# Kernel tuning notes

Hardware: AMD Instinct MI355X
Metric: run time of the kernel (lower is better)

Reference implementation:

```python
import jax, jax.numpy as jnp
import numpy as np

NUM_SECTORS = 11


def setup_inputs() -> dict:
    key = jax.random.key(0)
    k0, k1, k2, k3 = jax.random.split(key, 4)
    B, N, C, H = 4, 2048, 512, 8
    x = jax.random.normal(k0, (B, N, C), dtype=jnp.float32)
    w_qkv = jax.random.normal(k1, (C, 3 * C), dtype=jnp.float32) * 0.02
    w_proj = jax.random.normal(k2, (C, C), dtype=jnp.float32) * 0.02
    b_proj = jnp.zeros((C,), dtype=jnp.float32)
    gate_logit = jnp.full((H,), 2.0, dtype=jnp.float32)
    sector_ids = jax.random.randint(k3, (N,), 0, NUM_SECTORS, dtype=jnp.int64)
    return {"x": x, "w_qkv": w_qkv, "w_proj": w_proj, "b_proj": b_proj,
            "gate_logit": gate_logit, "sector_ids": sector_ids}


def reference(x, w_qkv, w_proj, b_proj, gate_logit, sector_ids):
    B, N, C = x.shape
    H = gate_logit.shape[0]
    d = C // H
    scale = d ** -0.5

    qkv = (x @ w_qkv).reshape(B, N, 3, H, d)
    qkv = jnp.transpose(qkv, (2, 0, 3, 1, 4))  # (3, B, H, N, d)
    q, k, v = qkv[0], qkv[1], qkv[2]

    # Content attention: softmax(QK^T / sqrt(d)) @ V
    attn = jnp.einsum('bhnd,bhmd->bhnm', q, k) * scale
    attn = jax.nn.softmax(attn, axis=-1)
    v_content = jnp.einsum('bhnm,bhmd->bhnd', attn, v)

    # Positional path: A_pos @ V == per-sector mean of V, gathered per row.
    # A_pos[i,j] = 1/|sector(i)| if sector(i)==sector(j); row_sum >= 1 always.
    ids = sector_ids.astype(jnp.int32)
    counts = jax.ops.segment_sum(jnp.ones((N,), x.dtype), ids, num_segments=NUM_SECTORS)
    counts = jnp.maximum(counts, 1.0)
    v_nfirst = jnp.transpose(v, (2, 0, 1, 3)).reshape(N, B * H * d)  # (N, BHd)
    sums = jax.ops.segment_sum(v_nfirst, ids, num_segments=NUM_SECTORS)  # (S, BHd)
    means = sums / counts[:, None]
    v_pos = means[ids].reshape(N, B, H, d).transpose(1, 2, 0, 3)  # (B, H, N, d)

    g = jax.nn.sigmoid(gate_logit)[None, :, None, None]
    out = g * v_pos + (1.0 - g) * v_content  # (B, H, N, d)
    out = jnp.transpose(out, (0, 2, 1, 3)).reshape(B, N, C)
    return out @ w_proj + b_proj
```

## Files before the change

kernel.cpp:

```cpp
#include <hip/hip_runtime.h>
#include <hip/hip_bf16.h>
#include <stdint.h>

typedef float f32x4 __attribute__((ext_vector_type(4)));
typedef float f32x16 __attribute__((ext_vector_type(16)));
typedef short bf16x8 __attribute__((ext_vector_type(8)));
typedef short short4v __attribute__((ext_vector_type(4)));
typedef int i32x4 __attribute__((ext_vector_type(4)));

#define MFMA16(a, b, c) __builtin_amdgcn_mfma_f32_16x16x32_bf16(a, b, c, 0, 0, 0)
#define MFMA32(a, b, c) __builtin_amdgcn_mfma_f32_32x32x16_bf16(a, b, c, 0, 0, 0)

__device__ __forceinline__ float bf2f(unsigned short u) {
    unsigned int x = ((unsigned int)u) << 16;
    float f;
    __builtin_memcpy(&f, &x, 4);
    return f;
}
__device__ __forceinline__ unsigned short f2bf(float f) {
    unsigned int x;
    __builtin_memcpy(&x, &f, 4);
    unsigned int r = x + 0x7FFFu + ((x >> 16) & 1u);
    return (unsigned short)(r >> 16);
}
__device__ __forceinline__ unsigned int cvt_pk_bf16(float lo, float hi) {
    unsigned int d;
    asm("v_cvt_pk_bf16_f32 %0, %1, %2" : "=v"(d) : "v"(lo), "v"(hi));
    return d;
}

#define GLD16(g, l)                                                        \
    __builtin_amdgcn_global_load_lds(                                      \
        (const __attribute__((address_space(1))) void*)(g),                \
        (__attribute__((address_space(3))) void*)(l), 16, 0, 0)

#define QSCALE 0.18033688011112042f

__global__ __launch_bounds__(256) void k_cvt_x(const float* __restrict__ x,
                                               unsigned short* __restrict__ xb) {
    int i = (blockIdx.x * 256 + threadIdx.x) * 4;
    float4 v = *(const float4*)(x + i);
    short4v o;
    o.x = (short)f2bf(v.x);
    o.y = (short)f2bf(v.y);
    o.z = (short)f2bf(v.z);
    o.w = (short)f2bf(v.w);
    *(short4v*)(xb + i) = o;
}

__global__ __launch_bounds__(256) void k_transpose_bf16(const float* __restrict__ in,
                                                        unsigned short* __restrict__ out,
                                                        int R, int C) {
    __shared__ float tile[32][33];
    int tx = threadIdx.x & 31, ty = threadIdx.x >> 5;
    int r0 = blockIdx.y * 32, c0 = blockIdx.x * 32;
#pragma unroll
    for (int i = 0; i < 32; i += 8) tile[ty + i][tx] = in[(r0 + ty + i) * C + c0 + tx];
    __syncthreads();
#pragma unroll
    for (int i = 0; i < 32; i += 8) out[(c0 + ty + i) * R + r0 + tx] = f2bf(tile[tx][ty + i]);
}

__global__ __launch_bounds__(256) void k_gemm_qkv(const unsigned short* __restrict__ A,
                                                  const unsigned short* __restrict__ Bt,
                                                  unsigned short* __restrict__ Q,
                                                  unsigned short* __restrict__ Kd,
                                                  unsigned short* __restrict__ Vt) {
    __shared__ alignas(16) unsigned short smem[128 * 128];
    unsigned short* As = smem;
    unsigned short* Bs = smem + 128 * 64;
    const int t = threadIdx.x;
    const int w = t >> 6, l = t & 63;
    const int brow = blockIdx.x * 128, bcol = blockIdx.y * 128;
    const int wr = (w >> 1) * 64, wc = (w & 1) * 64;
    const int li = l & 15, lk = (l >> 4) * 8;
    f32x4 acc[4][4] = {};

    for (int kt = 0; kt < 512; kt += 64) {
#pragma unroll
        for (int i = 0; i < 4; i++) {
            int ub = i * 256 + w * 64;
            int r = (ub >> 3) + (l >> 3);
            int ck = l & 7;
            GLD16(A + (brow + r) * 512 + kt + ck * 8, As + ub * 8);
            GLD16(Bt + (bcol + r) * 512 + kt + ck * 8, Bs + ub * 8);
        }
        __syncthreads();
#pragma unroll
        for (int ks = 0; ks < 2; ks++) {
            bf16x8 af[4], bfr[4];
#pragma unroll
            for (int m = 0; m < 4; m++)
                af[m] = *(const bf16x8*)(As + (wr + m * 16 + li) * 64 + ks * 32 + lk);
#pragma unroll
            for (int n = 0; n < 4; n++)
                bfr[n] = *(const bf16x8*)(Bs + (wc + n * 16 + li) * 64 + ks * 32 + lk);
#pragma unroll
            for (int m = 0; m < 4; m++)
#pragma unroll
                for (int n = 0; n < 4; n++)
                    acc[m][n] = MFMA16(af[m], bfr[n], acc[m][n]);
        }
        __syncthreads();
    }

    const int bb = brow >> 11, tok0 = brow & 2047;
    if (bcol < 1024) {
#pragma unroll
        for (int m = 0; m < 4; m++) {
#pragma unroll
            for (int n = 0; n < 4; n++) {
#pragma unroll
                for (int r = 0; r < 4; r++) {
                    int gm = brow + wr + m * 16 + (l >> 4) * 4 + r;
                    int gn = bcol + wc + n * 16 + li;
                    float v = acc[m][n][r];
                    int tok = gm & 2047;
                    int three = gn >> 9, hh = (gn >> 6) & 7, dd = gn & 63;
                    int bh = bb * 8 + hh;
                    if (three == 0)
                        Q[((bh << 11) + tok) * 64 + dd] = f2bf(v * QSCALE);
                    else
                        Kd[((bh << 11) + tok) * 64 + dd] = f2bf(v);
                }
            }
        }
    } else {
#pragma unroll
        for (int m = 0; m < 4; m++) {
#pragma unroll
            for (int n = 0; n < 4; n++) {
#pragma unroll
                for (int r = 0; r < 4; r++) {
                    int gnl = wc + n * 16 + li;
                    int gml = wr + m * 16 + (l >> 4) * 4 + r;
                    smem[gnl * 128 + (gml ^ ((gnl & 7) << 3))] = f2bf(acc[m][n][r]);
                }
            }
        }
        __syncthreads();
        int gnl = t >> 1, half = t & 1;
        int vcol = (bcol - 1024) + gnl;
        int hh = (vcol >> 6) & 7, dd = vcol & 63;
        unsigned short* dst = Vt + ((size_t)((bb * 8 + hh) * 64 + dd) << 11) + tok0 + half * 64;
#pragma unroll
        for (int j = 0; j < 8; j++) {
            int elem = (half * 64 + j * 8) ^ ((gnl & 7) << 3);
            *(bf16x8*)(dst + j * 8) = *(const bf16x8*)&smem[gnl * 128 + elem];
        }
    }
}

__global__ __launch_bounds__(256, 4) void k_attn(const unsigned short* __restrict__ Q,
                                                 const unsigned short* __restrict__ K,
                                                 const unsigned short* __restrict__ Vt,
                                                 const float* __restrict__ sums,
                                                 const float* __restrict__ invc,
                                                 const int* __restrict__ ids,
                                                 const float* __restrict__ gate,
                                                 unsigned short* __restrict__ mixb) {
    __shared__ alignas(16) unsigned short Ks[3][64 * 64];
    __shared__ alignas(16) unsigned short Vs[2][64 * 64];
    const int bid = blockIdx.x;
    const int bh = bid >> 5, qb = bid & 31;
    const int w = threadIdx.x >> 6, l = threadIdx.x & 63;
    const int wq = w >> 1, wk = w & 1;
    const int q = l & 31, hi = l >> 5;
    const unsigned short* Qh = Q + (size_t)bh * 2048 * 64;
    const char* Kb = (const char*)(K + (size_t)bh * 2048 * 64);
    const char* Vb = (const char*)(Vt + (size_t)bh * 64 * 2048);
    const int qbase = qb * 64 + wq * 32;
    const int swz = (q & 7) << 4;

    bf16x8 qf[4];
#pragma unroll
    for (int ks = 0; ks < 4; ks++)
        qf[ks] = *(const bf16x8*)(Qh + (qbase + q) * 64 + ks * 16 + hi * 8);

    f32x16 o0 = {}, o1 = {};
    float mx = -1e30f, sm = 0.f;

    auto stageK = [&](int buf, int kt) {
#pragma unroll
        for (int i = 0; i < 2; i++) {
            int abase = (w * 2 + i) * 1024;
            int al = abase + l * 16;
            int g = al ^ (((al >> 7) & 7) << 4);
            GLD16(Kb + (size_t)kt * 128 + g, (char*)Ks[buf] + abase);
        }
    };
    auto stageV = [&](int buf, int kt) {
#pragma unroll
        for (int i = 0; i < 2; i++) {
            int abase = (w * 2 + i) * 1024;
            int al = abase + l * 16;
            int row = al >> 7;
            int col = (al & 127) ^ ((row & 7) << 4);
            GLD16(Vb + (size_t)row * 4096 + kt * 2 + col, (char*)Vs[buf] + abase);
        }
    };

    stageK(0, 0);
    stageV(0, 0);
    stageK(1, 64);

#pragma unroll 1
    for (int it = 0; it < 32; ++it) {
        if (it < 31)
            asm volatile("s_waitcnt vmcnt(2)" ::: "memory");
        else
            asm volatile("s_waitcnt vmcnt(0)" ::: "memory");
        __builtin_amdgcn_sched_barrier(0);
        __builtin_amdgcn_s_barrier();
        __builtin_amdgcn_sched_barrier(0);

        if (it < 31) stageV((it + 1) & 1, (it + 1) * 64);
        __builtin_amdgcn_sched_barrier(0);
        if (it < 30) stageK((it + 2) % 3, (it + 2) * 64);

        const char* Kc = (const char*)Ks[it % 3];
        f32x16 s0 = {};
        __builtin_amdgcn_s_setprio(1);
#pragma unroll
        for (int ks = 0; ks < 4; ks++) {
            bf16x8 kf = *(const bf16x8*)(Kc + (wk * 32 + q) * 128 + ((ks * 32 + hi * 16) ^ swz));
            s0 = MFMA32(kf, qf[ks], s0);
        }
        __builtin_amdgcn_s_setprio(0);

        float c8[8];
#pragma unroll
        for (int r = 0; r < 8; r++) c8[r] = fmaxf(s0[r], s0[r + 8]);
#pragma unroll
        for (int r = 0; r < 4; r++) c8[r] = fmaxf(c8[r], c8[r + 4]);
        float tm = fmaxf(fmaxf(c8[0], c8[1]), fmaxf(c8[2], c8[3]));

        if (!__all(tm <= mx + 8.0f)) {
            float tmf = fmaxf(tm, __shfl_xor(tm, 32));
            float mn = fmaxf(mx, tmf);
            float fac = __builtin_amdgcn_exp2f(mx - mn);
            mx = mn;
#pragma unroll
            for (int r = 0; r < 16; r++) {
                o0[r] *= fac;
                o1[r] *= fac;
            }
            sm *= fac;
        }

        float a0 = 0.f, a1 = 0.f, a2 = 0.f, a3 = 0.f;
#pragma unroll
        for (int r = 0; r < 16; r += 4) {
            float p0 = __builtin_amdgcn_exp2f(s0[r] - mx);
            float p1 = __builtin_amdgcn_exp2f(s0[r + 1] - mx);
            float p2 = __builtin_amdgcn_exp2f(s0[r + 2] - mx);
            float p3 = __builtin_amdgcn_exp2f(s0[r + 3] - mx);
            s0[r] = p0;
            s0[r + 1] = p1;
            s0[r + 2] = p2;
            s0[r + 3] = p3;
            a0 += p0;
            a1 += p1;
            a2 += p2;
            a3 += p3;
        }
        sm += (a0 + a1) + (a2 + a3);

        unsigned int pk[4][2];
#pragma unroll
        for (int aa = 0; aa < 4; aa++)
#pragma unroll
            for (int c = 0; c < 2; c++)
                pk[aa][c] = cvt_pk_bf16(s0[4 * aa + 2 * c], s0[4 * aa + 2 * c + 1]);

        const char* Vc = (const char*)Vs[it & 1];
        __builtin_amdgcn_s_setprio(1);
#pragma unroll
        for (int ksl = 0; ksl < 2; ksl++) {
            unsigned int send0 = hi ? pk[2 * ksl][0] : pk[2 * ksl + 1][0];
            unsigned int send1 = hi ? pk[2 * ksl][1] : pk[2 * ksl + 1][1];
            unsigned int r0 = (unsigned int)__shfl_xor((int)send0, 32);
            unsigned int r1 = (unsigned int)__shfl_xor((int)send1, 32);
            unsigned int u0 = hi ? r0 : pk[2 * ksl][0];
            unsigned int u1 = hi ? r1 : pk[2 * ksl][1];
            unsigned int u2 = hi ? pk[2 * ksl + 1][0] : r0;
            unsigned int u3 = hi ? pk[2 * ksl + 1][1] : r1;
            i32x4 uu = {(int)u0, (int)u1, (int)u2, (int)u3};
            bf16x8 pa = __builtin_bit_cast(bf16x8, uu);
            int vcol = (wk * 64 + ksl * 32 + hi * 16);
            bf16x8 vf0 = *(const bf16x8*)(Vc + q * 128 + (vcol ^ swz));
            bf16x8 vf1 = *(const bf16x8*)(Vc + (q + 32) * 128 + (vcol ^ swz));
            o0 = MFMA32(pa, vf0, o0);
            o1 = MFMA32(pa, vf1, o1);
        }
        __builtin_amdgcn_s_setprio(0);
    }

    __syncthreads();

    sm = sm + __shfl_xor(sm, 32);

    float* So = ((float*)Ks) + wq * 2048;
    float* Sml = ((float*)Vs) + wq * 128;
    if (wk == 1) {
#pragma unroll
        for (int r = 0; r < 16; r++) {
            So[r * 64 + l] = o0[r];
            So[(16 + r) * 64 + l] = o1[r];
        }
        Sml[l] = mx;
        Sml[64 + l] = sm;
    }
    __syncthreads();
    if (wk == 0) {
        float m1 = Sml[l], l1 = Sml[64 + l];
        float ms = fmaxf(mx, m1);
        float f0 = __builtin_amdgcn_exp2f(mx - ms);
        float f1 = __builtin_amdgcn_exp2f(m1 - ms);
        float inv = 1.f / (f0 * sm + f1 * l1);
        float g = 1.f / (1.f + __expf(-gate[bh & 7]));
        float omg = 1.f - g;
        unsigned short* mrow = mixb + (size_t)(bh >> 3) * 2048 * 512 + (bh & 7) * 64;
#pragma unroll
        for (int r = 0; r < 16; r++) {
            float om0 = f0 * o0[r] + f1 * So[r * 64 + l];
            float om1 = f0 * o1[r] + f1 * So[(16 + r) * 64 + l];
            int qq = (r & 3) + 8 * (r >> 2) + 4 * hi;
            float iv = __shfl(inv, qq);
            int tok = qbase + qq;
            int sid = ids[tok];
            float ic = invc[sid];
            float vp0 = sums[((sid * 32 + bh) << 6) + q];
            float vp1 = sums[((sid * 32 + bh) << 6) + q + 32];
            mrow[(size_t)tok * 512 + q] = f2bf(g * vp0 * ic + omg * om0 * iv);
            mrow[(size_t)tok * 512 + q + 32] = f2bf(g * vp1 * ic + omg * om1 * iv);
        }
    }
}

__global__ void k_counts(const int* __restrict__ ids, float* __restrict__ invc) {
    __shared__ float h[11];
    int t = threadIdx.x;
    if (t < 11) h[t] = 0.f;
    __syncthreads();
    for (int n = t; n < 2048; n += 256) atomicAdd(&h[ids[n]], 1.0f);
    __syncthreads();
    if (t < 11) invc[t] = 1.f / fmaxf(h[t], 1.f);
}

__global__ __launch_bounds__(256) void k_sums(const unsigned short* __restrict__ Vt,
                                              const int* __restrict__ ids,
                                              float* __restrict__ sums) {
    __shared__ int ids_s[512];
    int bh = blockIdx.x, ch = blockIdx.y;
    int t = threadIdx.x;
    ids_s[t] = ids[ch * 512 + t];
    ids_s[t + 256] = ids[ch * 512 + 256 + t];
    __syncthreads();
    int dd = t & 63, sub = t >> 6;
    const unsigned short* row = Vt + ((size_t)(bh * 64 + dd) << 11) + ch * 512 + sub * 128;
    const int* idp = ids_s + sub * 128;
    float acc[11] = {};
    for (int i = 0; i < 128; i++) {
        float v = bf2f(row[i]);
        int s = idp[i];
#pragma unroll
        for (int si = 0; si < 11; si++) acc[si] += (s == si) ? v : 0.f;
    }
#pragma unroll
    for (int si = 0; si < 11; si++) atomicAdd(&sums[((si * 32 + bh) << 6) + dd], acc[si]);
}

__global__ __launch_bounds__(256) void k_gemm_out(const unsigned short* __restrict__ A,
                                                  const unsigned short* __restrict__ Bt,
                                                  const float* __restrict__ bias,
                                                  float* __restrict__ out) {
    __shared__ alignas(16) unsigned short As[64 * 64];
    __shared__ alignas(16) unsigned short Bs[128 * 64];
    const int t = threadIdx.x;
    const int w = t >> 6, l = t & 63;
    const int brow = blockIdx.x * 64, bcol = blockIdx.y * 128;
    const int wc = w * 32;
    const int li = l & 15, lk = (l >> 4) * 8;
    f32x4 acc[4][2] = {};

    for (int kt = 0; kt < 512; kt += 64) {
#pragma unroll
        for (int i = 0; i < 2; i++) {
            int ub = i * 256 + w * 64;
            int r = (ub >> 3) + (l >> 3);
            int ck = l & 7;
            GLD16(A + (brow + r) * 512 + kt + ck * 8, As + ub * 8);
        }
#pragma unroll
        for (int i = 0; i < 4; i++) {
            int ub = i * 256 + w * 64;
            int r = (ub >> 3) + (l >> 3);
            int ck = l & 7;
            GLD16(Bt + (bcol + r) * 512 + kt + ck * 8, Bs + ub * 8);
        }
        __syncthreads();
#pragma unroll
        for (int ks = 0; ks < 2; ks++) {
            bf16x8 af[4], bfr[2];
#pragma unroll
            for (int m = 0; m < 4; m++)
                af[m] = *(const bf16x8*)(As + (m * 16 + li) * 64 + ks * 32 + lk);
#pragma unroll
            for (int n = 0; n < 2; n++)
                bfr[n] = *(const bf16x8*)(Bs + (wc + n * 16 + li) * 64 + ks * 32 + lk);
#pragma unroll
            for (int m = 0; m < 4; m++)
#pragma unroll
                for (int n = 0; n < 2; n++)
                    acc[m][n] = MFMA16(af[m], bfr[n], acc[m][n]);
        }
        __syncthreads();
    }
#pragma unroll
    for (int m = 0; m < 4; m++) {
#pragma unroll
        for (int n = 0; n < 2; n++) {
#pragma unroll
            for (int r = 0; r < 4; r++) {
                int gm = brow + m * 16 + (l >> 4) * 4 + r;
                int gn = bcol + wc + n * 16 + li;
                out[(size_t)gm * 512 + gn] = acc[m][n][r] + bias[gn];
            }
        }
    }
}

extern "C" void kernel_launch(void* const* d_in, const int* in_sizes, int n_in,
                              void* d_out, int out_size, void* d_ws, size_t ws_size,
                              hipStream_t stream) {
    const float* x = (const float*)d_in[0];
    const float* w_qkv = (const float*)d_in[1];
    const float* w_proj = (const float*)d_in[2];
    const float* b_proj = (const float*)d_in[3];
    const float* gate = (const float*)d_in[4];
    const int* ids = (const int*)d_in[5];
    float* out = (float*)d_out;
    char* ws = (char*)d_ws;

    unsigned short* xb = (unsigned short*)(ws + 0);
    unsigned short* wqT = (unsigned short*)(ws + 8388608);
    unsigned short* wpT = (unsigned short*)(ws + 9961472);
    unsigned short* Q = (unsigned short*)(ws + 10485760);
    unsigned short* Kd = (unsigned short*)(ws + 18874368);
    unsigned short* Vt = (unsigned short*)(ws + 27262976);
    float* sums = (float*)(ws + 52428800);
    float* invc = (float*)(ws + 52518912);
    unsigned short* mixb = xb;

    hipMemsetAsync(ws + 52428800, 0, 90112 + 64, stream);

    k_cvt_x<<<4096, 256, 0, stream>>>(x, xb);
    {
        dim3 g(48, 16);
        k_transpose_bf16<<<g, 256, 0, stream>>>(w_qkv, wqT, 512, 1536);
    }
    {
        dim3 g(16, 16);
        k_transpose_bf16<<<g, 256, 0, stream>>>(w_proj, wpT, 512, 512);
    }
    {
        dim3 g(64, 12);
        k_gemm_qkv<<<g, 256, 0, stream>>>(xb, wqT, Q, Kd, Vt);
    }
    k_counts<<<1, 256, 0, stream>>>(ids, invc);
    {
        dim3 g(32, 4);
        k_sums<<<g, 256, 0, stream>>>(Vt, ids, sums);
    }
    k_attn<<<1024, 256, 0, stream>>>(Q, Kd, Vt, sums, invc, ids, gate, mixb);
    {
        dim3 g(128, 4);
        k_gemm_out<<<g, 256, 0, stream>>>(mixb, wpT, b_proj, out);
    }
}
```

Before: 199.7 us.

## Fuse preprocessing kernels, coalesce QK epilogue, swizzle attention blocks, use permlane swap

Merges the x conversion, both weight transposes and the sector-count kernel into one launch to cut launch overhead. The QKV GEMM epilogue for Q and K now stages tiles through swizzled shared memory and writes 16-byte rows instead of scattered 2-byte stores. The attention kernel remaps block ids so neighbouring blocks cover different heads, precomputes staging pointers, rotates buffer pointers, and replaces shuffles with v_permlane32_swap. k_sums gets more blocks and reduces in shared memory before the global atomics.

```diff
diff --git a/kernel.cpp b/kernel.cpp
--- a/kernel.cpp
+++ b/kernel.cpp
@@ -36,29 +36,51 @@
 
 #define QSCALE 0.18033688011112042f
 
-__global__ __launch_bounds__(256) void k_cvt_x(const float* __restrict__ x,
-                                               unsigned short* __restrict__ xb) {
-    int i = (blockIdx.x * 256 + threadIdx.x) * 4;
-    float4 v = *(const float4*)(x + i);
-    short4v o;
-    o.x = (short)f2bf(v.x);
-    o.y = (short)f2bf(v.y);
-    o.z = (short)f2bf(v.z);
-    o.w = (short)f2bf(v.w);
-    *(short4v*)(xb + i) = o;
-}
-
-__global__ __launch_bounds__(256) void k_transpose_bf16(const float* __restrict__ in,
-                                                        unsigned short* __restrict__ out,
-                                                        int R, int C) {
+__global__ __launch_bounds__(256) void k_pre(const float* __restrict__ x,
+                                             unsigned short* __restrict__ xb,
+                                             const float* __restrict__ w_qkv,
+                                             unsigned short* __restrict__ wqT,
+                                             const float* __restrict__ w_proj,
+                                             unsigned short* __restrict__ wpT,
+                                             const int* __restrict__ ids,
+                                             float* __restrict__ invc) {
     __shared__ float tile[32][33];
-    int tx = threadIdx.x & 31, ty = threadIdx.x >> 5;
-    int r0 = blockIdx.y * 32, c0 = blockIdx.x * 32;
-#pragma unroll
-    for (int i = 0; i < 32; i += 8) tile[ty + i][tx] = in[(r0 + ty + i) * C + c0 + tx];
-    __syncthreads();
-#pragma unroll
-    for (int i = 0; i < 32; i += 8) out[(c0 + ty + i) * R + r0 + tx] = f2bf(tile[tx][ty + i]);
+    __shared__ float h[11];
+    const int b = blockIdx.x, t = threadIdx.x;
+    if (b < 4096) {
+        int i = (b * 256 + t) * 4;
+        float4 v = *(const float4*)(x + i);
+        short4v o;
+        o.x = (short)f2bf(v.x);
+        o.y = (short)f2bf(v.y);
+        o.z = (short)f2bf(v.z);
+        o.w = (short)f2bf(v.w);
+        *(short4v*)(xb + i) = o;
+    } else if (b < 4096 + 768 + 256) {
+        const float* in;
+        unsigned short* out;
+        int R, C, bx, by;
+        if (b < 4096 + 768) {
+            int bb = b - 4096;
+            in = w_qkv; out = wqT; R = 512; C = 1536; bx = bb % 48; by = bb / 48;
+        } else {
+            int bb = b - 4096 - 768;
+            in = w_proj; out = wpT; R = 512; C = 512; bx = bb & 15; by = bb >> 4;
+        }
+        int tx = t & 31, ty = t >> 5;
+        int r0 = by * 32, c0 = bx * 32;
+#pragma unroll
+        for (int i = 0; i < 32; i += 8) tile[ty + i][tx] = in[(r0 + ty + i) * C + c0 + tx];
+        __syncthreads();
+#pragma unroll
+        for (int i = 0; i < 32; i += 8) out[(c0 + ty + i) * R + r0 + tx] = f2bf(tile[tx][ty + i]);
+    } else {
+        if (t < 11) h[t] = 0.f;
+        __syncthreads();
+        for (int n = t; n < 2048; n += 256) atomicAdd(&h[ids[n]], 1.0f);
+        __syncthreads();
+        if (t < 11) invc[t] = 1.f / fmaxf(h[t], 1.f);
+    }
 }
 
 __global__ __launch_bounds__(256) void k_gemm_qkv(const unsigned short* __restrict__ A,
@@ -106,38 +128,39 @@
 
     const int bb = brow >> 11, tok0 = brow & 2047;
     if (bcol < 1024) {
-#pragma unroll
-        for (int m = 0; m < 4; m++) {
-#pragma unroll
-            for (int n = 0; n < 4; n++) {
+        const float scl = (bcol < 512) ? QSCALE : 1.0f;
+#pragma unroll
+        for (int m = 0; m < 4; m++)
+#pragma unroll
+            for (int n = 0; n < 4; n++)
 #pragma unroll
                 for (int r = 0; r < 4; r++) {
-                    int gm = brow + wr + m * 16 + (l >> 4) * 4 + r;
-                    int gn = bcol + wc + n * 16 + li;
-                    float v = acc[m][n][r];
-                    int tok = gm & 2047;
-                    int three = gn >> 9, hh = (gn >> 6) & 7, dd = gn & 63;
-                    int bh = bb * 8 + hh;
-                    if (three == 0)
-                        Q[((bh << 11) + tok) * 64 + dd] = f2bf(v * QSCALE);
-                    else
-                        Kd[((bh << 11) + tok) * 64 + dd] = f2bf(v);
+                    int gml = wr + m * 16 + (l >> 4) * 4 + r;
+                    int gnl = wc + n * 16 + li;
+                    *(unsigned short*)((char*)smem + gml * 256 + ((gnl * 2) ^ ((gml & 7) << 4))) =
+                        f2bf(acc[m][n][r] * scl);
                 }
-            }
+        __syncthreads();
+        unsigned short* Tgt = (bcol < 512) ? Q : Kd;
+        int r = t >> 1, h2 = t & 1;
+        int hh = ((bcol >> 6) + h2) & 7;
+        unsigned short* dst = Tgt + ((size_t)(((bb * 8 + hh) << 11) + tok0 + r)) * 64;
+#pragma unroll
+        for (int j = 0; j < 8; j++) {
+            int boff = r * 256 + ((h2 * 128 + j * 16) ^ ((r & 7) << 4));
+            *(bf16x8*)(dst + j * 8) = *(const bf16x8*)((char*)smem + boff);
         }
     } else {
 #pragma unroll
-        for (int m = 0; m < 4; m++) {
-#pragma unroll
-            for (int n = 0; n < 4; n++) {
+        for (int m = 0; m < 4; m++)
+#pragma unroll
+            for (int n = 0; n < 4; n++)
 #pragma unroll
                 for (int r = 0; r < 4; r++) {
                     int gnl = wc + n * 16 + li;
                     int gml = wr + m * 16 + (l >> 4) * 4 + r;
                     smem[gnl * 128 + (gml ^ ((gnl & 7) << 3))] = f2bf(acc[m][n][r]);
                 }
-            }
-        }
         __syncthreads();
         int gnl = t >> 1, half = t & 1;
         int vcol = (bcol - 1024) + gnl;
@@ -161,7 +184,8 @@
                                                  unsigned short* __restrict__ mixb) {
     __shared__ alignas(16) unsigned short Ks[3][64 * 64];
     __shared__ alignas(16) unsigned short Vs[2][64 * 64];
-    const int bid = blockIdx.x;
+    const int rawbid = blockIdx.x;
+    const int bid = ((rawbid & 7) << 7) | (rawbid >> 3);
     const int bh = bid >> 5, qb = bid & 31;
     const int w = threadIdx.x >> 6, l = threadIdx.x & 63;
     const int wq = w >> 1, wk = w & 1;
@@ -180,29 +204,38 @@
     f32x16 o0 = {}, o1 = {};
     float mx = -1e30f, sm = 0.f;
 
-    auto stageK = [&](int buf, int kt) {
-#pragma unroll
-        for (int i = 0; i < 2; i++) {
-            int abase = (w * 2 + i) * 1024;
-            int al = abase + l * 16;
-            int g = al ^ (((al >> 7) & 7) << 4);
-            GLD16(Kb + (size_t)kt * 128 + g, (char*)Ks[buf] + abase);
-        }
+    const char *kp0, *kp1, *vp0, *vp1;
+    {
+        int ab0 = (w * 2) * 1024, al0 = ab0 + l * 16;
+        kp0 = Kb + (al0 ^ (((al0 >> 7) & 7) << 4));
+        int r0_ = al0 >> 7, c0_ = (al0 & 127) ^ ((r0_ & 7) << 4);
+        vp0 = Vb + (size_t)r0_ * 4096 + c0_;
+        int ab1 = ab0 + 1024, al1 = ab1 + l * 16;
+        kp1 = Kb + (al1 ^ (((al1 >> 7) & 7) << 4));
+        int r1_ = al1 >> 7, c1_ = (al1 & 127) ^ ((r1_ & 7) << 4);
+        vp1 = Vb + (size_t)r1_ * 4096 + c1_;
+    }
+    const int ab = (w * 2) * 1024;
+
+    auto stageK = [&](char* dst) {
+        GLD16(kp0, dst + ab);
+        GLD16(kp1, dst + ab + 1024);
+        kp0 += 8192;
+        kp1 += 8192;
     };
-    auto stageV = [&](int buf, int kt) {
-#pragma unroll
-        for (int i = 0; i < 2; i++) {
-            int abase = (w * 2 + i) * 1024;
-            int al = abase + l * 16;
-            int row = al >> 7;
-            int col = (al & 127) ^ ((row & 7) << 4);
-            GLD16(Vb + (size_t)row * 4096 + kt * 2 + col, (char*)Vs[buf] + abase);
-        }
+    auto stageV = [&](char* dst) {
+        GLD16(vp0, dst + ab);
+        GLD16(vp1, dst + ab + 1024);
+        vp0 += 128;
+        vp1 += 128;
     };
 
-    stageK(0, 0);
-    stageV(0, 0);
-    stageK(1, 64);
+    char *kc = (char*)Ks[0], *kn = (char*)Ks[1], *kf = (char*)Ks[2];
+    char *va = (char*)Vs[0], *vb2 = (char*)Vs[1];
+
+    stageK(kc);
+    stageV(va);
+    stageK(kn);
 
 #pragma unroll 1
     for (int it = 0; it < 32; ++it) {
@@ -214,17 +247,16 @@
         __builtin_amdgcn_s_barrier();
         __builtin_amdgcn_sched_barrier(0);
 
-        if (it < 31) stageV((it + 1) & 1, (it + 1) * 64);
+        if (it < 31) stageV(vb2);
         __builtin_amdgcn_sched_barrier(0);
-        if (it < 30) stageK((it + 2) % 3, (it + 2) * 64);
-
-        const char* Kc = (const char*)Ks[it % 3];
+        if (it < 30) stageK(kf);
+
         f32x16 s0 = {};
         __builtin_amdgcn_s_setprio(1);
 #pragma unroll
         for (int ks = 0; ks < 4; ks++) {
-            bf16x8 kf = *(const bf16x8*)(Kc + (wk * 32 + q) * 128 + ((ks * 32 + hi * 16) ^ swz));
-            s0 = MFMA32(kf, qf[ks], s0);
+            bf16x8 kfr = *(const bf16x8*)(kc + (wk * 32 + q) * 128 + ((ks * 32 + hi * 16) ^ swz));
+            s0 = MFMA32(kfr, qf[ks], s0);
         }
         __builtin_amdgcn_s_setprio(0);
 
@@ -273,27 +305,30 @@
             for (int c = 0; c < 2; c++)
                 pk[aa][c] = cvt_pk_bf16(s0[4 * aa + 2 * c], s0[4 * aa + 2 * c + 1]);
 
-        const char* Vc = (const char*)Vs[it & 1];
         __builtin_amdgcn_s_setprio(1);
 #pragma unroll
         for (int ksl = 0; ksl < 2; ksl++) {
-            unsigned int send0 = hi ? pk[2 * ksl][0] : pk[2 * ksl + 1][0];
-            unsigned int send1 = hi ? pk[2 * ksl][1] : pk[2 * ksl + 1][1];
-            unsigned int r0 = (unsigned int)__shfl_xor((int)send0, 32);
-            unsigned int r1 = (unsigned int)__shfl_xor((int)send1, 32);
-            unsigned int u0 = hi ? r0 : pk[2 * ksl][0];
-            unsigned int u1 = hi ? r1 : pk[2 * ksl][1];
-            unsigned int u2 = hi ? pk[2 * ksl + 1][0] : r0;
-            unsigned int u3 = hi ? pk[2 * ksl + 1][1] : r1;
-            i32x4 uu = {(int)u0, (int)u1, (int)u2, (int)u3};
+            unsigned int ua0 = pk[2 * ksl][0], ub0 = pk[2 * ksl + 1][0];
+            unsigned int ua1 = pk[2 * ksl][1], ub1 = pk[2 * ksl + 1][1];
+            asm volatile("v_permlane32_swap_b32 %0, %1" : "+v"(ua0), "+v"(ub0));
+            asm volatile("v_permlane32_swap_b32 %0, %1" : "+v"(ua1), "+v"(ub1));
+            i32x4 uu = {(int)ua0, (int)ua1, (int)ub0, (int)ub1};
             bf16x8 pa = __builtin_bit_cast(bf16x8, uu);
             int vcol = (wk * 64 + ksl * 32 + hi * 16);
-            bf16x8 vf0 = *(const bf16x8*)(Vc + q * 128 + (vcol ^ swz));
-            bf16x8 vf1 = *(const bf16x8*)(Vc + (q + 32) * 128 + (vcol ^ swz));
+            bf16x8 vf0 = *(const bf16x8*)(va + q * 128 + (vcol ^ swz));
+            bf16x8 vf1 = *(const bf16x8*)(va + (q + 32) * 128 + (vcol ^ swz));
             o0 = MFMA32(pa, vf0, o0);
             o1 = MFMA32(pa, vf1, o1);
         }
         __builtin_amdgcn_s_setprio(0);
+
+        char* tmp = kc;
+        kc = kn;
+        kn = kf;
+        kf = tmp;
+        tmp = va;
+        va = vb2;
+        vb2 = tmp;
     }
 
     __syncthreads();
@@ -338,37 +373,33 @@
     }
 }
 
-__global__ void k_counts(const int* __restrict__ ids, float* __restrict__ invc) {
-    __shared__ float h[11];
-    int t = threadIdx.x;
-    if (t < 11) h[t] = 0.f;
-    __syncthreads();
-    for (int n = t; n < 2048; n += 256) atomicAdd(&h[ids[n]], 1.0f);
-    __syncthreads();
-    if (t < 11) invc[t] = 1.f / fmaxf(h[t], 1.f);
-}
-
 __global__ __launch_bounds__(256) void k_sums(const unsigned short* __restrict__ Vt,
                                               const int* __restrict__ ids,
                                               float* __restrict__ sums) {
-    __shared__ int ids_s[512];
+    __shared__ int ids_s[128];
+    __shared__ float psum[11 * 64];
     int bh = blockIdx.x, ch = blockIdx.y;
     int t = threadIdx.x;
-    ids_s[t] = ids[ch * 512 + t];
-    ids_s[t + 256] = ids[ch * 512 + 256 + t];
+    for (int idx = t; idx < 704; idx += 256) psum[idx] = 0.f;
+    if (t < 128) ids_s[t] = ids[ch * 128 + t];
     __syncthreads();
     int dd = t & 63, sub = t >> 6;
-    const unsigned short* row = Vt + ((size_t)(bh * 64 + dd) << 11) + ch * 512 + sub * 128;
-    const int* idp = ids_s + sub * 128;
+    const unsigned short* row = Vt + ((size_t)(bh * 64 + dd) << 11) + ch * 128 + sub * 32;
+    const int* idp = ids_s + sub * 32;
     float acc[11] = {};
-    for (int i = 0; i < 128; i++) {
+    for (int i = 0; i < 32; i++) {
         float v = bf2f(row[i]);
         int s = idp[i];
 #pragma unroll
         for (int si = 0; si < 11; si++) acc[si] += (s == si) ? v : 0.f;
     }
 #pragma unroll
-    for (int si = 0; si < 11; si++) atomicAdd(&sums[((si * 32 + bh) << 6) + dd], acc[si]);
+    for (int si = 0; si < 11; si++) atomicAdd(&psum[si * 64 + dd], acc[si]);
+    __syncthreads();
+    for (int idx = t; idx < 704; idx += 256) {
+        int si = idx >> 6, d2 = idx & 63;
+        atomicAdd(&sums[((si * 32 + bh) << 6) + d2], psum[idx]);
+    }
 }
 
 __global__ __launch_bounds__(256) void k_gemm_out(const unsigned short* __restrict__ A,
@@ -455,22 +486,13 @@
 
     hipMemsetAsync(ws + 52428800, 0, 90112 + 64, stream);
 
-    k_cvt_x<<<4096, 256, 0, stream>>>(x, xb);
-    {
-        dim3 g(48, 16);
-        k_transpose_bf16<<<g, 256, 0, stream>>>(w_qkv, wqT, 512, 1536);
-    }
-    {
-        dim3 g(16, 16);
-        k_transpose_bf16<<<g, 256, 0, stream>>>(w_proj, wpT, 512, 512);
-    }
+    k_pre<<<5121, 256, 0, stream>>>(x, xb, w_qkv, wqT, w_proj, wpT, ids, invc);
     {
         dim3 g(64, 12);
         k_gemm_qkv<<<g, 256, 0, stream>>>(xb, wqT, Q, Kd, Vt);
     }
-    k_counts<<<1, 256, 0, stream>>>(ids, invc);
     {
-        dim3 g(32, 4);
+        dim3 g(32, 16);
         k_sums<<<g, 256, 0, stream>>>(Vt, ids, sums);
     }
     k_attn<<<1024, 256, 0, stream>>>(Q, Kd, Vt, sums, invc, ids, gate, mixb);
```

Result: faster. 190.6 us (-4.6%).
